# Performance work log

Measured on AMD Instinct MI355X. Metric: run time of the kernel, lower is better.

## Reference

```python
import jax, jax.numpy as jnp
import numpy as np

B, S, H, NH, NKV, HD, E, I = 1, 2048, 1024, 16, 8, 64, 8, 2048
TOPK = 2
EPS = 1e-6
THETA = 1e6


def setup_inputs() -> dict:
    key = jax.random.key(0)
    ks = jax.random.split(key, 12)
    init = lambda k, shp: jax.random.normal(k, shp, jnp.float32) * 0.02
    hidden_states = jax.random.normal(ks[0], (B, S, H), jnp.float32)
    attention_mask = jnp.ones((B, S), jnp.float32)
    position_ids = jnp.broadcast_to(jnp.arange(S, dtype=jnp.int32), (B, S))
    inv_freq = 1.0 / (THETA ** (jnp.arange(0, HD, 2, dtype=jnp.float32) / HD))
    freqs = jnp.outer(jnp.arange(S, dtype=jnp.float32), inv_freq)  # [S, HD/2]
    emb = jnp.concatenate([freqs, freqs], axis=-1)                  # [S, HD]
    return dict(
        hidden_states=hidden_states,
        attention_mask=attention_mask,
        position_ids=position_ids,
        sin=jnp.sin(emb), cos=jnp.cos(emb),
        wq=init(ks[1], (H, NH * HD)),
        wk=init(ks[2], (H, NKV * HD)),
        wv=init(ks[3], (H, NKV * HD)),
        wo=init(ks[4], (NH * HD, H)),
        ln1=jnp.ones((H,), jnp.float32),
        ln2=jnp.ones((H,), jnp.float32),
        gate_w=init(ks[5], (H, E)),
        w1=init(ks[6], (E, H, I)),
        w3=init(ks[7], (E, H, I)),
        w2=init(ks[8], (E, I, H)),
    )


def _rms_norm(x, w):
    return x * jax.lax.rsqrt(jnp.mean(jnp.square(x), -1, keepdims=True) + EPS) * w


def _rotate_half(x):
    h = x.shape[-1] // 2
    return jnp.concatenate([-x[..., h:], x[..., :h]], axis=-1)


def reference(hidden_states, attention_mask, position_ids, sin, cos,
              wq, wk, wv, wo, ln1, ln2, gate_w, w1, w3, w2):
    x = hidden_states
    # ---- self-attention block ----
    h = _rms_norm(x, ln1)
    q = (h @ wq).reshape(B, S, NH, HD).transpose(0, 2, 1, 3)    # [B,NH,S,HD]
    k = (h @ wk).reshape(B, S, NKV, HD).transpose(0, 2, 1, 3)   # [B,NKV,S,HD]
    v = (h @ wv).reshape(B, S, NKV, HD).transpose(0, 2, 1, 3)
    sb = sin[position_ids][:, None]  # [B,1,S,HD]
    cb = cos[position_ids][:, None]
    q = q * cb + _rotate_half(q) * sb
    k = k * cb + _rotate_half(k) * sb
    rep = NH // NKV
    k = jnp.repeat(k, rep, axis=1)  # GQA repeat -> [B,NH,S,HD]
    v = jnp.repeat(v, rep, axis=1)
    causal = jnp.tril(jnp.ones((S, S), bool))
    mask = causal[None, None] & (attention_mask[:, None, None, :] > 0)
    bias = jnp.where(mask, 0.0, jnp.finfo(jnp.float32).min)
    scale = 1.0 / jnp.sqrt(jnp.float32(HD))
    scores = jnp.einsum('bhqd,bhkd->bhqk', q, k) * scale + bias
    attn = jax.nn.softmax(scores, axis=-1)
    o = jnp.einsum('bhqk,bhkd->bhqd', attn, v)
    o = o.transpose(0, 2, 1, 3).reshape(B, S, NH * HD) @ wo
    x = x + o
    # ---- sparse MoE block (top-2 of E experts, SiLU-gated MLP) ----
    t = _rms_norm(x, ln2).reshape(B * S, H)
    router_logits = t @ gate_w                         # [T,E]
    probs = jax.nn.softmax(router_logits, axis=-1)
    top_w, top_i = jax.lax.top_k(probs, TOPK)          # [T,2]
    top_w = top_w / jnp.sum(top_w, axis=-1, keepdims=True)
    full_w = jnp.sum(jax.nn.one_hot(top_i, E, dtype=t.dtype) * top_w[..., None], axis=1)  # [T,E]
    moe_out = jnp.zeros_like(t)
    for e in range(E):  # fixed small expert count
        ge = jax.nn.silu(t @ w1[e]) * (t @ w3[e])      # [T,I]
        moe_out = moe_out + full_w[:, e:e + 1] * (ge @ w2[e])
    x = x + moe_out.reshape(B, S, H)
    return x
```

## Files before the change

### kernel.cpp

```cpp
#include <hip/hip_runtime.h>

#define S 2048
#define H 1024
#define NH 16
#define NKV 8
#define HD 64
#define NE 8
#define ID 2048

typedef short bf16x8 __attribute__((ext_vector_type(8)));
typedef short bf16x4 __attribute__((ext_vector_type(4)));
typedef float f32x4 __attribute__((ext_vector_type(4)));

__device__ __forceinline__ unsigned short f2bf(float f) {
  unsigned u = __builtin_bit_cast(unsigned, f);
  u += 0x7FFFu + ((u >> 16) & 1u);
  return (unsigned short)(u >> 16);
}
__device__ __forceinline__ float bf2f(unsigned short h) {
  unsigned u = ((unsigned)h) << 16;
  return __builtin_bit_cast(float, u);
}
__device__ __forceinline__ unsigned cvtpk(float a, float b) {
  unsigned r;
// ... 17 lines not shown
  const float* sb = src + (size_t)(kt * 128) * N + nt * 64 + ln;
#pragma unroll 8
  for (int rr = 0; rr < 32; rr++) {
    int r = rr * 4 + wv;
    tile[r][ln] = sb[(size_t)r * N];
  }
  __syncthreads();
  int seg = tid & 15;
  int rq = tid >> 4;
#pragma unroll
  for (int it = 0; it < 4; it++) {
    int row = it * 16 + rq;
    int cs = seg * 8;
    size_t dbase = (size_t)(nt * 64 + row) * K + kt * 128 + cs;
    unsigned short th[8], tl[8];
#pragma unroll
    for (int i = 0; i < 8; i++) {
      float vv = tile[cs + i][row];
      unsigned short h_ = f2bf(vv);
      th[i] = h_;
      if (LO) tl[i] = f2bf(vv - bf2f(h_));
    }
    *(bf16x8*)(hi + dbase) = *(bf16x8*)&th[0];
    if (LO) *(bf16x8*)(lo + dbase) = *(bf16x8*)&tl[0];
  }
}

__global__ __launch_bounds__(256) void prep_kernel(
    const float* __restrict__ x, const float* __restrict__ ln1,
    unsigned short* __restrict__ h_hi, unsigned short* __restrict__ h_lo,
    const float* __restrict__ wq, const float* __restrict__ wk, const float* __restrict__ wv,
    const float* __restrict__ wo, unsigned short* __restrict__ wqkvT_hi,
    unsigned short* __restrict__ wqkvT_lo, unsigned short* __restrict__ woT_hi,
    unsigned short* __restrict__ woT_lo) {
  __shared__ float tile[128][65];
  __shared__ float part[4];
  int u = blockIdx.x, grp = u / 19, slot = u % 19;
  int tid = threadIdx.x;
  if (slot < 16) {
    int row = grp * 16 + slot;
    const float* xr = x + (size_t)row * H;
    float v[4];
    float ss = 0.f;
#pragma unroll
    for (int i = 0; i < 4; i++) {
      v[i] = xr[tid + i * 256];
      ss += v[i] * v[i];
    }
#pragma unroll
    for (int off = 1; off < 64; off <<= 1) ss += __shfl_xor(ss, off);
    if ((tid & 63) == 0) part[tid >> 6] = ss;
    __syncthreads();
    float tot = part[0] + part[1] + part[2] + part[3];
    float r = rsqrtf(tot * (1.f / H) + 1e-6f);
#pragma unroll
    for (int i = 0; i < 4; i++) {
      int c = tid + i * 256;
      float vv = v[i] * r * ln1[c];
      size_t o = (size_t)row * H + c;
      unsigned short h_ = f2bf(vv);
      h_hi[o] = h_;
      h_lo[o] = f2bf(vv - bf2f(h_));
    }
  } else {
    int local = grp * 3 + (slot - 16);
    const float* src;
    unsigned short *hi, *lo;
    int N, l2;
    if (local < 128) {
      src = wq; hi = wqkvT_hi; lo = wqkvT_lo; N = 1024; l2 = local;
    } else if (local < 192) {
      src = wk; hi = wqkvT_hi + (size_t)1024 * 1024; lo = wqkvT_lo + (size_t)1024 * 1024; N = 512; l2 = local - 128;
    } else if (local < 256) {
      src = wv; hi = wqkvT_hi + (size_t)1536 * 1024; lo = wqkvT_lo + (size_t)1536 * 1024; N = 512; l2 = local - 192;
    } else {
      src = wo; hi = woT_hi; lo = woT_lo; N = 1024; l2 = local - 256;
    }
    int ntc = N >> 6;
    int nt = l2 % ntc, kt = l2 / ntc;
    tconv_tile128<true>(src, hi, lo, 1024, N, nt, kt, tile);
  }
}

__global__ __launch_bounds__(256) void rv_kernel(
    const float* __restrict__ qkv, const float* __restrict__ sinb,
    const float* __restrict__ cosb, const int* __restrict__ pos,
    unsigned short* __restrict__ qhi, unsigned short* __restrict__ qlo,
    unsigned short* __restrict__ khi, unsigned short* __restrict__ klo,
    unsigned short* __restrict__ vThi, unsigned short* __restrict__ vTlo) {
  __shared__ float tile[64][65];
  int u = blockIdx.x, grp = u / 25, slot = u % 25;
  int tid = threadIdx.x;
  if (slot == 0) {
    int st = grp & 31, hk = grp >> 5;
    int r = tid >> 2, seg = (tid & 3) * 16;
    const float* src = qkv + (size_t)(st * 64 + r) * 2048 + 1536 + hk * HD + seg;
#pragma unroll
    for (int i = 0; i < 16; i += 4) {
      float4 a = *(const float4*)(src + i);
      tile[r][seg + i] = a.x;
      tile[r][seg + i + 1] = a.y;
      tile[r][seg + i + 2] = a.z;
      tile[r][seg + i + 3] = a.w;
    }
    __syncthreads();
    int d = tid >> 2, ss = (tid & 3) * 16;
    unsigned short th[16], tl[16];
#pragma unroll
    for (int i = 0; i < 16; i++) {
      float vv = tile[ss + i][d];
      unsigned short h_ = f2bf(vv);
      th[i] = h_;
      tl[i] = f2bf(vv - bf2f(h_));
    }
    size_t dst = ((size_t)hk * HD + d) * S + st * 64 + ss;
    *(bf16x8*)(vThi + dst) = *(bf16x8*)&th[0];
    *(bf16x8*)(vThi + dst + 8) = *(bf16x8*)&th[8];
    *(bf16x8*)(vTlo + dst) = *(bf16x8*)&tl[0];
    *(bf16x8*)(vTlo + dst + 8) = *(bf16x8*)&tl[8];
  } else {
    int i = (grp * 24 + slot - 1) * 256 + tid;
    int d = i & 31;
    int s = (i >> 5) & 2047;
    int hh = i >> 16;
    int p = pos[s];
    float c0 = cosb[p * HD + d], c1 = cosb[p * HD + d + 32];
    float s0 = sinb[p * HD + d], s1 = sinb[p * HD + d + 32];
    const float* srcb = qkv + (size_t)s * 2048;
    if (hh < NH) {
      float x0 = srcb[hh * HD + d], x1 = srcb[hh * HD + d + 32];
      float r0 = (x0 * c0 - x1 * s0) * 0.125f;
      float r1 = (x1 * c1 + x0 * s1) * 0.125f;
      size_t o = ((size_t)hh * S + s) * HD + d;
      unsigned short h0 = f2bf(r0), h1 = f2bf(r1);
      qhi[o] = h0;
      qlo[o] = f2bf(r0 - bf2f(h0));
      qhi[o + 32] = h1;
      qlo[o + 32] = f2bf(r1 - bf2f(h1));
    } else {
      int hk = hh - NH;
      float x0 = srcb[1024 + hk * HD + d], x1 = srcb[1024 + hk * HD + d + 32];
      float r0 = x0 * c0 - x1 * s0;
      float r1 = x1 * c1 + x0 * s1;
      size_t o = ((size_t)hk * S + s) * HD + d;
      unsigned short h0 = f2bf(r0), h1 = f2bf(r1);
      khi[o] = h0;
      klo[o] = f2bf(r0 - bf2f(h0));
      khi[o + 32] = h1;
      klo[o + 32] = f2bf(r1 - bf2f(h1));
    }
  }
}

__global__ __launch_bounds__(256, 4) void gemm1_w13_kernel(
    const unsigned short* __restrict__ oh, const unsigned short* __restrict__ ol,
    const unsigned short* __restrict__ woh, const unsigned short* __restrict__ wol,
    float* __restrict__ x2, float* __restrict__ out, const float* __restrict__ resid,
    const float* __restrict__ w1, const float* __restrict__ w3,
    unsigned short* __restrict__ w1T, unsigned short* __restrict__ w3T) {
  __shared__ __align__(16) char smem[33280];
  int u = blockIdx.x, grp = u / 9, slot = u % 9;
  int tid = threadIdx.x;
  if (slot != 0) {
    int t = grp * 8 + slot - 1;
    int b = t >> 8, rem = t & 255, kt = rem >> 5, nt = rem & 31;
    const float* src = (b < 8) ? w1 + (size_t)b * 1024 * 2048 : w3 + (size_t)(b - 8) * 1024 * 2048;
    unsigned short* hi = (b < 8) ? w1T + (size_t)b * 2048 * 1024 : w3T + (size_t)(b - 8) * 2048 * 1024;
    tconv_tile128<false>(src, hi, nullptr, 1024, 2048, nt, kt, (float(*)[65])smem);
    return;
  }
  int g = grp;
  int bx = g & 15, by = g >> 4;
  unsigned short* tAh = (unsigned short*)smem;
  unsigned short* tAl = tAh + 4096;
  unsigned short* tBh = tAl + 4096;
  unsigned short* tBl = tBh + 4096;
  int n0 = bx * 64, m0 = by * 64;
  int w = tid >> 6, lane = tid & 63;
  int lr = lane & 15, gq = lane >> 4;
  int rloc = lane >> 3, slotg = (lane & 7) ^ rloc;
  int wm = w >> 1, wn = w & 1;
  unsigned aOff[2], bOff[2];
#pragma unroll
  for (int cc = 0; cc < 2; cc++) {
    int rr = (w * 2 + cc) * 8 + rloc;
    aOff[cc] = (unsigned)((m0 + rr) * 1024 + slotg * 8);
    bOff[cc] = (unsigned)((n0 + rr) * 1024 + slotg * 8);
  }
  f32x4 acc[2][2];
#pragma unroll
  for (int i = 0; i < 2; i++)
#pragma unroll
    for (int j = 0; j < 2; j++) acc[i][j] = f32x4{0.f, 0.f, 0.f, 0.f};
  for (int k0 = 0; k0 < 1024; k0 += 64) {
    __syncthreads();
#pragma unroll
    for (int cc = 0; cc < 2; cc++) {
      int cb = (w * 2 + cc) * 512;
      gload16(oh + aOff[cc] + k0, &tAh[cb]);
      gload16(ol + aOff[cc] + k0, &tAl[cb]);
      gload16(woh + bOff[cc] + k0, &tBh[cb]);
      gload16(wol + bOff[cc] + k0, &tBl[cb]);
    }
    __syncthreads();
    bf16x8 fah[2][2], fal[2][2];
#pragma unroll
    for (int i = 0; i < 2; i++) {
      int ar = wm * 32 + i * 16 + lr;
#pragma unroll
      for (int kk = 0; kk < 2; kk++) {
        int off = ar * 64 + (((kk * 4 + gq) ^ (ar & 7)) * 8);
        fah[i][kk] = *(const bf16x8*)&tAh[off];
        fal[i][kk] = *(const bf16x8*)&tAl[off];
      }
    }
#pragma unroll
    for (int j = 0; j < 2; j++) {
      int br = wn * 32 + j * 16 + lr;
      bf16x8 fbh[2], fbl[2];
#pragma unroll
      for (int kk = 0; kk < 2; kk++) {
        int off = br * 64 + (((kk * 4 + gq) ^ (br & 7)) * 8);
        fbh[kk] = *(const bf16x8*)&tBh[off];
        fbl[kk] = *(const bf16x8*)&tBl[off];
      }
#pragma unroll
      for (int i = 0; i < 2; i++) {
#pragma unroll
        for (int kk = 0; kk < 2; kk++) {
          acc[i][j] = __builtin_amdgcn_mfma_f32_16x16x32_bf16(fah[i][kk], fbh[kk], acc[i][j], 0, 0, 0);
          acc[i][j] = __builtin_amdgcn_mfma_f32_16x16x32_bf16(fah[i][kk], fbl[kk], acc[i][j], 0, 0, 0);
          acc[i][j] = __builtin_amdgcn_mfma_f32_16x16x32_bf16(fal[i][kk], fbh[kk], acc[i][j], 0, 0, 0);
        }
      }
    }
  }
#pragma unroll
  for (int i = 0; i < 2; i++)
#pragma unroll
    for (int j = 0; j < 2; j++)
#pragma unroll
      for (int r = 0; r < 4; r++) {
        int grow = wm * 32 + i * 16 + gq * 4 + r;
        int gcol = n0 + wn * 32 + j * 16 + lr;
        float o = acc[i][j][r] + resid[(size_t)(m0 + grow) * 1024 + gcol];
        x2[(size_t)(m0 + grow) * 1024 + gcol] = o;
        out[(size_t)(m0 + grow) * 1024 + gcol] = o;
      }
}

__global__ __launch_bounds__(256) void rmsnorm_router_kernel(
    const float* __restrict__ x, const float* __restrict__ wgt,
    const float* __restrict__ gw, unsigned short* __restrict__ ohi,
    int* __restrict__ selE, float* __restrict__ selW) {
  int row = blockIdx.x;
  const float* xr = x + (size_t)row * H;
  int tid = threadIdx.x;
  float v[4];
  float ss = 0.f;
#pragma unroll
  for (int i = 0; i < 4; i++) {
    v[i] = xr[tid + i * 256];
    ss += v[i] * v[i];
  }
#pragma unroll
  for (int off = 1; off < 64; off <<= 1) ss += __shfl_xor(ss, off);
  __shared__ float part[4];
  __shared__ float red[4][NE];
  if ((tid & 63) == 0) part[tid >> 6] = ss;
  __syncthreads();
  float tot = part[0] + part[1] + part[2] + part[3];
  float r = rsqrtf(tot * (1.f / H) + 1e-6f);
  float acc[NE];
#pragma unroll
  for (int e = 0; e < NE; e++) acc[e] = 0.f;
#pragma unroll
  for (int i = 0; i < 4; i++) {
    int c = tid + i * 256;
    float vv = v[i] * r * wgt[c];
    ohi[(size_t)row * H + c] = f2bf(vv);
    const float4* gp = (const float4*)(gw + (size_t)c * NE);
    float4 g0 = gp[0], g1 = gp[1];
    acc[0] += vv * g0.x;
    acc[1] += vv * g0.y;
    acc[2] += vv * g0.z;
    acc[3] += vv * g0.w;
    acc[4] += vv * g1.x;
    acc[5] += vv * g1.y;
    acc[6] += vv * g1.z;
    acc[7] += vv * g1.w;
  }
#pragma unroll
  for (int off = 1; off < 64; off <<= 1) {
#pragma unroll
    for (int e = 0; e < NE; e++) acc[e] += __shfl_xor(acc[e], off);
  }
  if ((tid & 63) == 0) {
#pragma unroll
    for (int e = 0; e < NE; e++) red[tid >> 6][e] = acc[e];
  }
  __syncthreads();
  if (tid == 0) {
    float lg[NE];
#pragma unroll
    for (int e = 0; e < NE; e++) lg[e] = red[0][e] + red[1][e] + red[2][e] + red[3][e];
    int e1 = 0;
#pragma unroll
    for (int e = 1; e < NE; e++)
      if (lg[e] > lg[e1]) e1 = e;
    int e2 = -1;
#pragma unroll
    for (int e = 0; e < NE; e++)
      if (e != e1 && (e2 < 0 || lg[e] > lg[e2])) e2 = e;
    float w1v = 1.f / (1.f + __expf(lg[e2] - lg[e1]));
    selE[row] = e1 | (e2 << 8);
    selW[row * 2] = w1v;
    selW[row * 2 + 1] = 1.f - w1v;
  }
}

__global__ __launch_bounds__(256) void assign_kernel(const int* __restrict__ selE,
                                                     int* __restrict__ cnt,
                                                     int* __restrict__ offs,
                                                     int* __restrict__ tmap,
                                                     int* __restrict__ idxb,
                                                     int* __restrict__ tokslot) {
  int tid = threadIdx.x;
  __shared__ int sc[256][NE];
  int pack[8];
// ... 94 lines not shown
template <int MODE>
__global__ __launch_bounds__(256, 4) void gemm_kernel(
    const unsigned short* __restrict__ Ah, const unsigned short* __restrict__ Al,
    const unsigned short* __restrict__ Bh, const unsigned short* __restrict__ Bl,
    float* __restrict__ C, unsigned short* __restrict__ Gout,
    const int* __restrict__ idx, const int* __restrict__ cnt, const int* __restrict__ offs,
    const int* __restrict__ tmap, int N, int K) {
  constexpr int BM = (MODE <= 1) ? 64 : 128;
  constexpr int NI = BM / 32;
  int n0 = blockIdx.x * 64, m0, e = 0;
  int ce = 0, gbase = 0;
  if (MODE >= 2) {
    int ntiles = tmap[63];
    if ((int)blockIdx.y >= ntiles) return;
    int packed = tmap[blockIdx.y];
    e = packed >> 16;
    m0 = (packed & 0xffff) * 128;
    ce = cnt[e];
    gbase = offs[e];
  } else {
    m0 = blockIdx.y * BM;
  }
  const unsigned short* bhp = Bh;
  const unsigned short* blp = Bl;
  if (MODE == 2) {
    bhp += (size_t)e * 2048 * 1024;
    blp += (size_t)e * 2048 * 1024;
  }
  if (MODE == 3) bhp += (size_t)e * 1024 * 2048;

  __shared__ __align__(16) unsigned short tAh[BM * 64];
  __shared__ __align__(16) unsigned short tAl[MODE <= 1 ? BM * 64 : 8];
  __shared__ __align__(16) unsigned short tBh[64 * 64];
  __shared__ __align__(16) unsigned short tBl[MODE <= 2 ? 64 * 64 : 8];

  int tid = threadIdx.x, w = tid >> 6, lane = tid & 63;
  int lr = lane & 15, g = lane >> 4;
  int rloc = lane >> 3, slotg = (lane & 7) ^ rloc;
  int wm = w >> 1, wn = w & 1;

  unsigned aOff[NI], bOff[2];
#pragma unroll
  for (int cc = 0; cc < NI; cc++) {
    int rr = (w * NI + cc) * 8 + rloc;
    if (MODE == 2) {
      int gr = m0 + rr;
      if (gr > ce - 1) gr = ce - 1;
      int tok = idx[e * S + gr];
      aOff[cc] = (unsigned)(tok * K + slotg * 8);
    } else if (MODE == 3) {
      int gr = gbase + m0 + rr;
      if (gr > 4095) gr = 4095;
      aOff[cc] = (unsigned)(gr * K + slotg * 8);
    } else {
      aOff[cc] = (unsigned)((m0 + rr) * K + slotg * 8);
    }
  }
#pragma unroll
  for (int cc = 0; cc < 2; cc++) {
    int rr = (w * 2 + cc) * 8 + rloc;
    bOff[cc] = (unsigned)((n0 + rr) * K + slotg * 8);
  }

  f32x4 acc[NI][2], acc2[NI][2];
#pragma unroll
  for (int i = 0; i < NI; i++)
#pragma unroll
    for (int j = 0; j < 2; j++) {
      acc[i][j] = f32x4{0.f, 0.f, 0.f, 0.f};
      if (MODE == 2) acc2[i][j] = f32x4{0.f, 0.f, 0.f, 0.f};
    }

  int kbeg = 0, kend = K;
  if (MODE == 3) {
    kbeg = (int)blockIdx.z * (K >> 1);
    kend = kbeg + (K >> 1);
  }
  for (int k0 = kbeg; k0 < kend; k0 += 64) {
    __syncthreads();
#pragma unroll
    for (int cc = 0; cc < NI; cc++) {
      int cb = (w * NI + cc) * 512;
      gload16(Ah + aOff[cc] + k0, &tAh[cb]);
      if (MODE <= 1) gload16(Al + aOff[cc] + k0, &tAl[cb]);
    }
#pragma unroll
    for (int cc = 0; cc < 2; cc++) {
      int cb = (w * 2 + cc) * 512;
      gload16(bhp + bOff[cc] + k0, &tBh[cb]);
      if (MODE <= 2) gload16(blp + bOff[cc] + k0, &tBl[cb]);
    }
    __syncthreads();
    bf16x8 fah[NI][2], fal[NI][2];
#pragma unroll
    for (int i = 0; i < NI; i++) {
      int ar = wm * (BM / 2) + i * 16 + lr;
#pragma unroll
      for (int kk = 0; kk < 2; kk++) {
        int off = ar * 64 + (((kk * 4 + g) ^ (ar & 7)) * 8);
        fah[i][kk] = *(const bf16x8*)&tAh[off];
        if (MODE <= 1) fal[i][kk] = *(const bf16x8*)&tAl[off];
      }
    }
#pragma unroll
    for (int j = 0; j < 2; j++) {
      int br = wn * 32 + j * 16 + lr;
      bf16x8 fbh[2], fbl[2];
#pragma unroll
      for (int kk = 0; kk < 2; kk++) {
        int off = br * 64 + (((kk * 4 + g) ^ (br & 7)) * 8);
        fbh[kk] = *(const bf16x8*)&tBh[off];
        if (MODE <= 2) fbl[kk] = *(const bf16x8*)&tBl[off];
      }
#pragma unroll
      for (int i = 0; i < NI; i++) {
#pragma unroll
        for (int kk = 0; kk < 2; kk++) {
          acc[i][j] = __builtin_amdgcn_mfma_f32_16x16x32_bf16(fah[i][kk], fbh[kk], acc[i][j], 0, 0, 0);
          if (MODE <= 1) {
            acc[i][j] = __builtin_amdgcn_mfma_f32_16x16x32_bf16(fah[i][kk], fbl[kk], acc[i][j], 0, 0, 0);
            acc[i][j] = __builtin_amdgcn_mfma_f32_16x16x32_bf16(fal[i][kk], fbh[kk], acc[i][j], 0, 0, 0);
          }
          if (MODE == 2)
            acc2[i][j] = __builtin_amdgcn_mfma_f32_16x16x32_bf16(fah[i][kk], fbl[kk], acc2[i][j], 0, 0, 0);
        }
      }
    }
  }
#pragma unroll
  for (int i = 0; i < NI; i++)
#pragma unroll
    for (int j = 0; j < 2; j++)
#pragma unroll
      for (int r = 0; r < 4; r++) {
        int grow = wm * (BM / 2) + i * 16 + g * 4 + r;
        int gcol = n0 + wn * 32 + j * 16 + lr;
        float v = acc[i][j][r];
        if (MODE == 0) {
          C[(size_t)(m0 + grow) * N + gcol] = v;
        } else if (MODE == 2) {
          if (m0 + grow < ce) {
            float g3 = acc2[i][j][r];
            float sg = v / (1.f + __expf(-v));
            Gout[(size_t)(gbase + m0 + grow) * 2048 + gcol] = f2bf(sg * g3);
          }
        } else if (MODE == 3) {
          if (m0 + grow < ce) {
            C[(size_t)blockIdx.z * 4096 * 1024 + (size_t)(gbase + m0 + grow) * 1024 + gcol] = v;
          }
        }
      }
}

#define FSWZ(row, byteoff) ((byteoff) ^ (((row) & 7) << 4))

__global__ __launch_bounds__(256, 4) void flash_kernel(
    const unsigned short* __restrict__ qhi, const unsigned short* __restrict__ qlo,
    const unsigned short* __restrict__ khip, const unsigned short* __restrict__ klop,
    const unsigned short* __restrict__ vthip, const unsigned short* __restrict__ vtlop,
    const float* __restrict__ amask, float* __restrict__ po, float* __restrict__ pm,
    float* __restrict__ pl) {
  int u = blockIdx.x;
  int r_ = u >> 8, base = u & 255;
  int qt = (base + r_ * 8) & 31;
  int head = ((base >> 5) & 7) | ((r_ & 1) << 3);
  int z = r_ >> 1;
  int tid = threadIdx.x;
  int w = tid >> 6, lane = tid & 63;
  int lr = lane & 15, g = lane >> 4;
  int rloc = lane >> 3, slotg = (lane & 7) ^ rloc;

  __shared__ __align__(16) unsigned short Khi[64 * 64];
  __shared__ __align__(16) unsigned short Klo[64 * 64];
  __shared__ __align__(16) unsigned short Vhi[64 * 64];
  __shared__ __align__(16) unsigned short Vlo[64 * 64];
  __shared__ __align__(16) unsigned short Pbuf[4][16 * 64];

  int qrow = qt * 64 + w * 16 + lr;
  bf16x8 qh[2], ql[2];
  {
    const unsigned short* qb = qhi + ((size_t)head * S + qrow) * HD;
    const unsigned short* qb2 = qlo + ((size_t)head * S + qrow) * HD;
    qh[0] = *(const bf16x8*)(qb + g * 8);
    qh[1] = *(const bf16x8*)(qb + 32 + g * 8);
    ql[0] = *(const bf16x8*)(qb2 + g * 8);
    ql[1] = *(const bf16x8*)(qb2 + 32 + g * 8);
  }

  f32x4 oacc[4];
#pragma unroll
  for (int dg = 0; dg < 4; dg++) oacc[dg] = f32x4{0.f, 0.f, 0.f, 0.f};
  float m = -1e30f, l = 0.f;

  const unsigned short* kbh = khip + (size_t)(head >> 1) * S * HD;
  const unsigned short* kbl = klop + (size_t)(head >> 1) * S * HD;
  const unsigned short* vbh = vthip + (size_t)(head >> 1) * HD * S;
  const unsigned short* vbl = vtlop + (size_t)(head >> 1) * HD * S;
  char* pbase = (char*)Pbuf[w];

  int nblk = qt + 1;
  int b0 = (z * nblk) >> 1, b1 = ((z + 1) * nblk) >> 1;

  for (int kb = b0; kb < b1; kb++) {
    int kv0 = kb * 64;
    __syncthreads();
#pragma unroll
    for (int cc = 0; cc < 2; cc++) {
      int c = w * 2 + cc;
      int r = c * 8 + rloc;
      gload16(kbh + (size_t)(kv0 + r) * HD + slotg * 8, &Khi[c * 512]);
      gload16(kbl + (size_t)(kv0 + r) * HD + slotg * 8, &Klo[c * 512]);
      gload16(vbh + (size_t)r * S + kv0 + slotg * 8, &Vhi[c * 512]);
      gload16(vbl + (size_t)r * S + kv0 + slotg * 8, &Vlo[c * 512]);
    }
    unsigned long long vm = __ballot(amask[kv0 + lane] > 0.f);
    __syncthreads();

    f32x4 sacc[4];
#pragma unroll
    for (int c = 0; c < 4; c++) sacc[c] = f32x4{0.f, 0.f, 0.f, 0.f};
#pragma unroll
    for (int c = 0; c < 4; c++) {
#pragma unroll
      for (int kc = 0; kc < 2; kc++) {
        int row = c * 16 + lr;
        int bo = FSWZ(row, row * 128 + kc * 64 + g * 16);
        bf16x8 khf = *(const bf16x8*)((char*)Khi + bo);
        bf16x8 klf = *(const bf16x8*)((char*)Klo + bo);
        sacc[c] = __builtin_amdgcn_mfma_f32_16x16x32_bf16(khf, qh[kc], sacc[c], 0, 0, 0);
        sacc[c] = __builtin_amdgcn_mfma_f32_16x16x32_bf16(khf, ql[kc], sacc[c], 0, 0, 0);
        sacc[c] = __builtin_amdgcn_mfma_f32_16x16x32_bf16(klf, qh[kc], sacc[c], 0, 0, 0);
      }
    }
    int qloc = w * 16 + lr;
    bool diag = (kb == qt);
    bool fullvis = (vm == ~0ull) && !diag;
    float tm = -1e30f;
    if (fullvis) {
#pragma unroll
      for (int c = 0; c < 4; c++)
#pragma unroll
        for (int r = 0; r < 4; r++) tm = fmaxf(tm, sacc[c][r]);
    } else {
#pragma unroll
      for (int c = 0; c < 4; c++) {
#pragma unroll
        for (int r = 0; r < 4; r++) {
          int kvloc = c * 16 + 4 * g + r;
          bool vis = ((vm >> kvloc) & 1ull) && (!diag || kvloc <= qloc);
          float sv = vis ? sacc[c][r] : -1e30f;
          sacc[c][r] = sv;
          tm = fmaxf(tm, sv);
        }
      }
    }
    tm = fmaxf(tm, __shfl_xor(tm, 16));
    tm = fmaxf(tm, __shfl_xor(tm, 32));
    bool skip = __all(tm - m <= 8.f);
    float newm = skip ? m : fmaxf(m, tm);
    float rs = 0.f;
#pragma unroll
    for (int c = 0; c < 4; c++) {
#pragma unroll
      for (int r = 0; r < 4; r++) {
        float p = __expf(sacc[c][r] - newm);
        sacc[c][r] = p;
        rs += p;
      }
    }
    rs += __shfl_xor(rs, 16);
    rs += __shfl_xor(rs, 32);
    if (!skip) {
      float alpha = __expf(m - newm);
      m = newm;
      l = l * alpha + rs;
#pragma unroll
      for (int dg = 0; dg < 4; dg++) {
#pragma unroll
        for (int r = 0; r < 4; r++) oacc[dg][r] *= alpha;
      }
    } else {
      l += rs;
    }
    unsigned hw[4][2];
#pragma unroll
    for (int c = 0; c < 4; c++) {
      hw[c][0] = cvtpk(sacc[c][0], sacc[c][1]);
      hw[c][1] = cvtpk(sacc[c][2], sacc[c][3]);
      uint2 hv = {hw[c][0], hw[c][1]};
      *(uint2*)(pbase + FSWZ(lr, lr * 128 + (c * 16 + 4 * g) * 2)) = hv;
    }
    bf16x8 pbh[2], pbl[2];
#pragma unroll
    for (int kc = 0; kc < 2; kc++)
      pbh[kc] = *(const bf16x8*)(pbase + FSWZ(lr, lr * 128 + kc * 64 + g * 16));
#pragma unroll
    for (int c = 0; c < 4; c++) {
      float h0 = __builtin_bit_cast(float, hw[c][0] << 16);
      float h1 = __builtin_bit_cast(float, hw[c][0] & 0xffff0000u);
      float h2 = __builtin_bit_cast(float, hw[c][1] << 16);
      float h3 = __builtin_bit_cast(float, hw[c][1] & 0xffff0000u);
      uint2 lv = {cvtpk(sacc[c][0] - h0, sacc[c][1] - h1),
                  cvtpk(sacc[c][2] - h2, sacc[c][3] - h3)};
      *(uint2*)(pbase + FSWZ(lr, lr * 128 + (c * 16 + 4 * g) * 2)) = lv;
    }
#pragma unroll
    for (int kc = 0; kc < 2; kc++)
      pbl[kc] = *(const bf16x8*)(pbase + FSWZ(lr, lr * 128 + kc * 64 + g * 16));
#pragma unroll
    for (int dg = 0; dg < 4; dg++) {
#pragma unroll
      for (int kc = 0; kc < 2; kc++) {
        int row = dg * 16 + lr;
        int bo = FSWZ(row, row * 128 + kc * 64 + g * 16);
        bf16x8 vhf = *(const bf16x8*)((char*)Vhi + bo);
        bf16x8 vlf = *(const bf16x8*)((char*)Vlo + bo);
        oacc[dg] = __builtin_amdgcn_mfma_f32_16x16x32_bf16(vhf, pbh[kc], oacc[dg], 0, 0, 0);
        oacc[dg] = __builtin_amdgcn_mfma_f32_16x16x32_bf16(vhf, pbl[kc], oacc[dg], 0, 0, 0);
        oacc[dg] = __builtin_amdgcn_mfma_f32_16x16x32_bf16(vlf, pbh[kc], oacc[dg], 0, 0, 0);
      }
    }
  }

  size_t pb = (size_t)(qt * 16 + head) * 2 + z;
  int row = w * 16 + lr;
  if (g == 0) {
    pm[pb * 64 + row] = m;
    pl[pb * 64 + row] = l;
  }
  float* pob = po + pb * 4096 + (size_t)row * 64;
#pragma unroll
  for (int dg = 0; dg < 4; dg++) {
    float4 v4 = {oacc[dg][0], oacc[dg][1], oacc[dg][2], oacc[dg][3]};
    *(float4*)(pob + dg * 16 + 4 * g) = v4;
  }
}

__global__ __launch_bounds__(256) void combine_kernel(const float* __restrict__ po,
                                                      const float* __restrict__ pm,
                                                      const float* __restrict__ pl,
                                                      unsigned short* __restrict__ ohi,
                                                      unsigned short* __restrict__ olo) {
  int qt = blockIdx.x, head = blockIdx.y;
  int r = threadIdx.x >> 2, dg = (threadIdx.x & 3) * 16;
  size_t base = (size_t)(qt * 16 + head) * 2;
  float m0v = pm[base * 64 + r], m1v = pm[(base + 1) * 64 + r];
  float l0 = pl[base * 64 + r], l1 = pl[(base + 1) * 64 + r];
  float M = fmaxf(m0v, m1v);
  float w0 = __expf(m0v - M), w1 = __expf(m1v - M);
  float inv = 1.f / (w0 * l0 + w1 * l1);
  const float* p0 = po + base * 4096 + (size_t)r * 64 + dg;
  const float* p1 = po + (base + 1) * 4096 + (size_t)r * 64 + dg;
  unsigned short th[16], tl[16];
#pragma unroll
  for (int i = 0; i < 16; i += 4) {
    float4 a = *(const float4*)(p0 + i);
    float4 b = *(const float4*)(p1 + i);
    float vv[4] = {(w0 * a.x + w1 * b.x) * inv, (w0 * a.y + w1 * b.y) * inv,
                   (w0 * a.z + w1 * b.z) * inv, (w0 * a.w + w1 * b.w) * inv};
#pragma unroll
    for (int j = 0; j < 4; j++) {
      unsigned short h_ = f2bf(vv[j]);
      th[i + j] = h_;
      tl[i + j] = f2bf(vv[j] - bf2f(h_));
    }
  }
  size_t ob = (size_t)(qt * 64 + r) * 1024 + head * 64 + dg;
  *(bf16x8*)(ohi + ob) = *(bf16x8*)&th[0];
  *(bf16x8*)(ohi + ob + 8) = *(bf16x8*)&th[8];
  *(bf16x8*)(olo + ob) = *(bf16x8*)&tl[0];
  *(bf16x8*)(olo + ob + 8) = *(bf16x8*)&tl[8];
}

extern "C" void kernel_launch(void* const* d_in, const int* in_sizes, int n_in,
                              void* d_out, int out_size, void* d_ws, size_t ws_size,
                              hipStream_t stream) {
  const float* x = (const float*)d_in[0];
  const float* amask = (const float*)d_in[1];
  const int* pos = (const int*)d_in[2];
  const float* sinb = (const float*)d_in[3];
  const float* cosb = (const float*)d_in[4];
  const float* wq = (const float*)d_in[5];
  const float* wk = (const float*)d_in[6];
  const float* wv = (const float*)d_in[7];
  const float* wo = (const float*)d_in[8];
  const float* ln1 = (const float*)d_in[9];
  const float* ln2 = (const float*)d_in[10];
  const float* gw = (const float*)d_in[11];
  const float* w1 = (const float*)d_in[12];
  const float* w3 = (const float*)d_in[13];
  const float* w2 = (const float*)d_in[14];
  float* out = (float*)d_out;

  char* ws = (char*)d_ws;
  const size_t MB = 1024 * 1024;
  float* x2 = (float*)(ws + 0 * MB);
  unsigned short* t_bf = (unsigned short*)(ws + 8 * MB);
  int* cnt = (int*)(ws + 12 * MB);
  int* offs = cnt + 16;
  int* tmap = cnt + 32;
  int* idxb = cnt + 128;
  int* selE = idxb + 16384;
  int* tokslot = selE + 2048;
  float* selW = (float*)(tokslot + 4096);
  unsigned short* o_hi = (unsigned short*)(ws + 13 * MB);
  unsigned short* o_lo = (unsigned short*)(ws + 17 * MB);
  unsigned short* G = (unsigned short*)(ws + 13 * MB);
  float* qkv = (float*)(ws + 13 * MB);
  unsigned short* w1T = (unsigned short*)(ws + 29 * MB);
  unsigned short* w3T = (unsigned short*)(ws + 61 * MB);
  unsigned short* w2T = (unsigned short*)(ws + 29 * MB);
  float* moeP = (float*)(ws + 61 * MB);
  float* po = (float*)(ws + 29 * MB);
  float* pm = (float*)(ws + 45 * MB);
  float* pl = (float*)(ws + 46 * MB);
  unsigned short* wqkvT_hi = (unsigned short*)(ws + 47 * MB);
  unsigned short* wqkvT_lo = (unsigned short*)(ws + 51 * MB);
  unsigned short* h_hi = (unsigned short*)(ws + 55 * MB);
  unsigned short* h_lo = (unsigned short*)(ws + 59 * MB);
  unsigned short* q_hi = (unsigned short*)(ws + 63 * MB);
  unsigned short* q_lo = (unsigned short*)(ws + 67 * MB);
  unsigned short* k_hi = (unsigned short*)(ws + 71 * MB);
  unsigned short* k_lo = (unsigned short*)(ws + 73 * MB);
  unsigned short* vT_hi = (unsigned short*)(ws + 75 * MB);
  unsigned short* vT_lo = (unsigned short*)(ws + 77 * MB);
  unsigned short* woT_hi = (unsigned short*)(ws + 93 * MB);
  unsigned short* woT_lo = (unsigned short*)(ws + 95 * MB);

  prep_kernel<<<2432, 256, 0, stream>>>(x, ln1, h_hi, h_lo, wq, wk, wv, wo, wqkvT_hi, wqkvT_lo,
                                        woT_hi, woT_lo);
  gemm_kernel<0><<<dim3(32, 32, 1), 256, 0, stream>>>(h_hi, h_lo, wqkvT_hi, wqkvT_lo, qkv, nullptr,
                                                      nullptr, nullptr, nullptr, nullptr, 2048,
                                                      1024);
  rv_kernel<<<6400, 256, 0, stream>>>(qkv, sinb, cosb, pos, q_hi, q_lo, k_hi, k_lo, vT_hi, vT_lo);
  flash_kernel<<<dim3(1024, 1, 1), 256, 0, stream>>>(q_hi, q_lo, k_hi, k_lo, vT_hi, vT_lo, amask,
                                                     po, pm, pl);
  combine_kernel<<<dim3(32, 16), 256, 0, stream>>>(po, pm, pl, o_hi, o_lo);
  gemm1_w13_kernel<<<4608, 256, 0, stream>>>(o_hi, o_lo, woT_hi, woT_lo, x2, out, x, w1, w3, w1T,
                                             w3T);
  rmsnorm_router_kernel<<<S, 256, 0, stream>>>(x2, ln2, gw, t_bf, selE, selW);
  assign_kernel<<<1, 256, 0, stream>>>(selE, cnt, offs, tmap, idxb, tokslot);
  gemm_kernel<2><<<dim3(32, 40, 1), 256, 0, stream>>>(t_bf, nullptr, w1T, w3T, nullptr, G, idxb,
                                                      cnt, offs, tmap, 2048, 1024);
  tconv_w2_kernel<<<dim3(16, 16, 8), 256, 0, stream>>>(w2, w2T);
  gemm_kernel<3><<<dim3(16, 40, 2), 256, 0, stream>>>(G, nullptr, w2T, nullptr, moeP, nullptr,
                                                      idxb, cnt, offs, tmap, 1024, 2048);
  moe_gather_kernel<<<S, 256, 0, stream>>>(moeP, tokslot, selW, out);
}
```

Before: 281.3 us.

## Co-schedule w1/w3 weight transpose with flash attention instead of output GEMM

Moves the w1/w3 fp32-to-bf16 transpose tiles out of the output-projection GEMM launch and interleaves them with flash-attention blocks (4 transpose blocks per attention block). The goal is to fill idle CU time from causal-attention imbalance with memory-bound conversion work, leaving the Wo GEMM as a lean 512-block launch. The workspace is remapped so w1T/w3T no longer overlap the attention partials. The attention MFMA loops also gain s_setprio hints. The risk is that the bandwidth-heavy transpose competes with attention's loads and that the shared-memory footprint per block grows.

```diff
diff --git a/kernel.cpp b/kernel.cpp
--- a/kernel.cpp
+++ b/kernel.cpp
@@ -193,29 +193,215 @@
   }
 }
 
-__global__ __launch_bounds__(256, 4) void gemm1_w13_kernel(
-    const unsigned short* __restrict__ oh, const unsigned short* __restrict__ ol,
-    const unsigned short* __restrict__ woh, const unsigned short* __restrict__ wol,
-    float* __restrict__ x2, float* __restrict__ out, const float* __restrict__ resid,
-    const float* __restrict__ w1, const float* __restrict__ w3,
+#define FSWZ(row, byteoff) ((byteoff) ^ (((row) & 7) << 4))
+
+__global__ __launch_bounds__(256, 4) void flash_w13_kernel(
+    const unsigned short* __restrict__ qhi, const unsigned short* __restrict__ qlo,
+    const unsigned short* __restrict__ khip, const unsigned short* __restrict__ klop,
+    const unsigned short* __restrict__ vthip, const unsigned short* __restrict__ vtlop,
+    const float* __restrict__ amask, float* __restrict__ po, float* __restrict__ pm,
+    float* __restrict__ pl, const float* __restrict__ w1, const float* __restrict__ w3,
     unsigned short* __restrict__ w1T, unsigned short* __restrict__ w3T) {
-  __shared__ __align__(16) char smem[33280];
-  int u = blockIdx.x, grp = u / 9, slot = u % 9;
+  __shared__ __align__(16) char smem[40960];
+  int uu = blockIdx.x, grp = uu / 5, slot = uu % 5;
   int tid = threadIdx.x;
   if (slot != 0) {
-    int t = grp * 8 + slot - 1;
+    int t = grp * 4 + slot - 1;
     int b = t >> 8, rem = t & 255, kt = rem >> 5, nt = rem & 31;
     const float* src = (b < 8) ? w1 + (size_t)b * 1024 * 2048 : w3 + (size_t)(b - 8) * 1024 * 2048;
     unsigned short* hi = (b < 8) ? w1T + (size_t)b * 2048 * 1024 : w3T + (size_t)(b - 8) * 2048 * 1024;
     tconv_tile128<false>(src, hi, nullptr, 1024, 2048, nt, kt, (float(*)[65])smem);
     return;
   }
-  int g = grp;
+  unsigned short* Khi = (unsigned short*)smem;
+  unsigned short* Klo = Khi + 4096;
+  unsigned short* Vhi = Klo + 4096;
+  unsigned short* Vlo = Vhi + 4096;
+  unsigned short* Pbuf = Vlo + 4096;
+  int u = grp;
+  int r_ = u >> 8, base = u & 255;
+  int qt = (base + r_ * 8) & 31;
+  int head = ((base >> 5) & 7) | ((r_ & 1) << 3);
+  int z = r_ >> 1;
+  int w = tid >> 6, lane = tid & 63;
+  int lr = lane & 15, g = lane >> 4;
+  int rloc = lane >> 3, slotg = (lane & 7) ^ rloc;
+
+  int qrow = qt * 64 + w * 16 + lr;
+  bf16x8 qh[2], ql[2];
+  {
+    const unsigned short* qb = qhi + ((size_t)head * S + qrow) * HD;
+    const unsigned short* qb2 = qlo + ((size_t)head * S + qrow) * HD;
+    qh[0] = *(const bf16x8*)(qb + g * 8);
+    qh[1] = *(const bf16x8*)(qb + 32 + g * 8);
+    ql[0] = *(const bf16x8*)(qb2 + g * 8);
+    ql[1] = *(const bf16x8*)(qb2 + 32 + g * 8);
+  }
+
+  f32x4 oacc[4];
+#pragma unroll
+  for (int dg = 0; dg < 4; dg++) oacc[dg] = f32x4{0.f, 0.f, 0.f, 0.f};
+  float m = -1e30f, l = 0.f;
+
+  const unsigned short* kbh = khip + (size_t)(head >> 1) * S * HD;
+  const unsigned short* kbl = klop + (size_t)(head >> 1) * S * HD;
+  const unsigned short* vbh = vthip + (size_t)(head >> 1) * HD * S;
+  const unsigned short* vbl = vtlop + (size_t)(head >> 1) * HD * S;
+  char* pbase = (char*)(Pbuf + w * 1024);
+
+  int nblk = qt + 1;
+  int b0 = (z * nblk) >> 1, b1 = ((z + 1) * nblk) >> 1;
+
+  for (int kb = b0; kb < b1; kb++) {
+    int kv0 = kb * 64;
+    __syncthreads();
+#pragma unroll
+    for (int cc = 0; cc < 2; cc++) {
+      int c = w * 2 + cc;
+      int r = c * 8 + rloc;
+      gload16(kbh + (size_t)(kv0 + r) * HD + slotg * 8, &Khi[c * 512]);
+      gload16(kbl + (size_t)(kv0 + r) * HD + slotg * 8, &Klo[c * 512]);
+      gload16(vbh + (size_t)r * S + kv0 + slotg * 8, &Vhi[c * 512]);
+      gload16(vbl + (size_t)r * S + kv0 + slotg * 8, &Vlo[c * 512]);
+    }
+    unsigned long long vm = __ballot(amask[kv0 + lane] > 0.f);
+    __syncthreads();
+
+    f32x4 sacc[4];
+#pragma unroll
+    for (int c = 0; c < 4; c++) sacc[c] = f32x4{0.f, 0.f, 0.f, 0.f};
+    __builtin_amdgcn_s_setprio(1);
+#pragma unroll
+    for (int c = 0; c < 4; c++) {
+#pragma unroll
+      for (int kc = 0; kc < 2; kc++) {
+        int row = c * 16 + lr;
+        int bo = FSWZ(row, row * 128 + kc * 64 + g * 16);
+        bf16x8 khf = *(const bf16x8*)((char*)Khi + bo);
+        bf16x8 klf = *(const bf16x8*)((char*)Klo + bo);
+        sacc[c] = __builtin_amdgcn_mfma_f32_16x16x32_bf16(khf, qh[kc], sacc[c], 0, 0, 0);
+        sacc[c] = __builtin_amdgcn_mfma_f32_16x16x32_bf16(khf, ql[kc], sacc[c], 0, 0, 0);
+        sacc[c] = __builtin_amdgcn_mfma_f32_16x16x32_bf16(klf, qh[kc], sacc[c], 0, 0, 0);
+      }
+    }
+    __builtin_amdgcn_s_setprio(0);
+    int qloc = w * 16 + lr;
+    bool diag = (kb == qt);
+    bool fullvis = (vm == ~0ull) && !diag;
+    float tm = -1e30f;
+    if (fullvis) {
+#pragma unroll
+      for (int c = 0; c < 4; c++)
+#pragma unroll
+        for (int r = 0; r < 4; r++) tm = fmaxf(tm, sacc[c][r]);
+    } else {
+#pragma unroll
+      for (int c = 0; c < 4; c++) {
+#pragma unroll
+        for (int r = 0; r < 4; r++) {
+          int kvloc = c * 16 + 4 * g + r;
+          bool vis = ((vm >> kvloc) & 1ull) && (!diag || kvloc <= qloc);
+          float sv = vis ? sacc[c][r] : -1e30f;
+          sacc[c][r] = sv;
+          tm = fmaxf(tm, sv);
+        }
+      }
+    }
+    tm = fmaxf(tm, __shfl_xor(tm, 16));
+    tm = fmaxf(tm, __shfl_xor(tm, 32));
+    bool skip = __all(tm - m <= 8.f);
+    float newm = skip ? m : fmaxf(m, tm);
+    float rs = 0.f;
+#pragma unroll
+    for (int c = 0; c < 4; c++) {
+#pragma unroll
+      for (int r = 0; r < 4; r++) {
+        float p = __expf(sacc[c][r] - newm);
+        sacc[c][r] = p;
+        rs += p;
+      }
+    }
+    rs += __shfl_xor(rs, 16);
+    rs += __shfl_xor(rs, 32);
+    if (!skip) {
+      float alpha = __expf(m - newm);
+      m = newm;
+      l = l * alpha + rs;
+#pragma unroll
+      for (int dg = 0; dg < 4; dg++) {
+#pragma unroll
+        for (int r = 0; r < 4; r++) oacc[dg][r] *= alpha;
+      }
+    } else {
+      l += rs;
+    }
+    unsigned hw[4][2];
+#pragma unroll
+    for (int c = 0; c < 4; c++) {
+      hw[c][0] = cvtpk(sacc[c][0], sacc[c][1]);
+      hw[c][1] = cvtpk(sacc[c][2], sacc[c][3]);
+      uint2 hv = {hw[c][0], hw[c][1]};
+      *(uint2*)(pbase + FSWZ(lr, lr * 128 + (c * 16 + 4 * g) * 2)) = hv;
+    }
+    bf16x8 pbh[2], pbl[2];
+#pragma unroll
+    for (int kc = 0; kc < 2; kc++)
+      pbh[kc] = *(const bf16x8*)(pbase + FSWZ(lr, lr * 128 + kc * 64 + g * 16));
+#pragma unroll
+    for (int c = 0; c < 4; c++) {
+      float h0 = __builtin_bit_cast(float, hw[c][0] << 16);
+      float h1 = __builtin_bit_cast(float, hw[c][0] & 0xffff0000u);
+      float h2 = __builtin_bit_cast(float, hw[c][1] << 16);
+      float h3 = __builtin_bit_cast(float, hw[c][1] & 0xffff0000u);
+      uint2 lv = {cvtpk(sacc[c][0] - h0, sacc[c][1] - h1),
+                  cvtpk(sacc[c][2] - h2, sacc[c][3] - h3)};
+      *(uint2*)(pbase + FSWZ(lr, lr * 128 + (c * 16 + 4 * g) * 2)) = lv;
+    }
+#pragma unroll
+    for (int kc = 0; kc < 2; kc++)
+      pbl[kc] = *(const bf16x8*)(pbase + FSWZ(lr, lr * 128 + kc * 64 + g * 16));
+    __builtin_amdgcn_s_setprio(1);
+#pragma unroll
+    for (int dg = 0; dg < 4; dg++) {
+#pragma unroll
+      for (int kc = 0; kc < 2; kc++) {
+        int row = dg * 16 + lr;
+        int bo = FSWZ(row, row * 128 + kc * 64 + g * 16);
+        bf16x8 vhf = *(const bf16x8*)((char*)Vhi + bo);
+        bf16x8 vlf = *(const bf16x8*)((char*)Vlo + bo);
+        oacc[dg] = __builtin_amdgcn_mfma_f32_16x16x32_bf16(vhf, pbh[kc], oacc[dg], 0, 0, 0);
+        oacc[dg] = __builtin_amdgcn_mfma_f32_16x16x32_bf16(vhf, pbl[kc], oacc[dg], 0, 0, 0);
+        oacc[dg] = __builtin_amdgcn_mfma_f32_16x16x32_bf16(vlf, pbh[kc], oacc[dg], 0, 0, 0);
+      }
+    }
+    __builtin_amdgcn_s_setprio(0);
+  }
+
+  size_t pb = (size_t)(qt * 16 + head) * 2 + z;
+  int row = w * 16 + lr;
+  if (g == 0) {
+    pm[pb * 64 + row] = m;
+    pl[pb * 64 + row] = l;
+  }
+  float* pob = po + pb * 4096 + (size_t)row * 64;
+#pragma unroll
+  for (int dg = 0; dg < 4; dg++) {
+    float4 v4 = {oacc[dg][0], oacc[dg][1], oacc[dg][2], oacc[dg][3]};
+    *(float4*)(pob + dg * 16 + 4 * g) = v4;
+  }
+}
+
+__global__ __launch_bounds__(256, 4) void gemm1_kernel(
+    const unsigned short* __restrict__ oh, const unsigned short* __restrict__ ol,
+    const unsigned short* __restrict__ woh, const unsigned short* __restrict__ wol,
+    float* __restrict__ x2, float* __restrict__ out, const float* __restrict__ resid) {
+  __shared__ __align__(16) unsigned short tAh[4096];
+  __shared__ __align__(16) unsigned short tAl[4096];
+  __shared__ __align__(16) unsigned short tBh[4096];
+  __shared__ __align__(16) unsigned short tBl[4096];
+  int g = blockIdx.x;
   int bx = g & 15, by = g >> 4;
-  unsigned short* tAh = (unsigned short*)smem;
-  unsigned short* tAl = tAh + 4096;
-  unsigned short* tBh = tAl + 4096;
-  unsigned short* tBl = tBh + 4096;
+  int tid = threadIdx.x;
   int n0 = bx * 64, m0 = by * 64;
   int w = tid >> 6, lane = tid & 63;
   int lr = lane & 15, gq = lane >> 4;
@@ -616,190 +802,6 @@
       }
 }
 
-#define FSWZ(row, byteoff) ((byteoff) ^ (((row) & 7) << 4))
-
-__global__ __launch_bounds__(256, 4) void flash_kernel(
-    const unsigned short* __restrict__ qhi, const unsigned short* __restrict__ qlo,
-    const unsigned short* __restrict__ khip, const unsigned short* __restrict__ klop,
-    const unsigned short* __restrict__ vthip, const unsigned short* __restrict__ vtlop,
-    const float* __restrict__ amask, float* __restrict__ po, float* __restrict__ pm,
-    float* __restrict__ pl) {
-  int u = blockIdx.x;
-  int r_ = u >> 8, base = u & 255;
-  int qt = (base + r_ * 8) & 31;
-  int head = ((base >> 5) & 7) | ((r_ & 1) << 3);
-  int z = r_ >> 1;
-  int tid = threadIdx.x;
-  int w = tid >> 6, lane = tid & 63;
-  int lr = lane & 15, g = lane >> 4;
-  int rloc = lane >> 3, slotg = (lane & 7) ^ rloc;
-
-  __shared__ __align__(16) unsigned short Khi[64 * 64];
-  __shared__ __align__(16) unsigned short Klo[64 * 64];
-  __shared__ __align__(16) unsigned short Vhi[64 * 64];
-  __shared__ __align__(16) unsigned short Vlo[64 * 64];
-  __shared__ __align__(16) unsigned short Pbuf[4][16 * 64];
-
-  int qrow = qt * 64 + w * 16 + lr;
-  bf16x8 qh[2], ql[2];
-  {
-    const unsigned short* qb = qhi + ((size_t)head * S + qrow) * HD;
-    const unsigned short* qb2 = qlo + ((size_t)head * S + qrow) * HD;
-    qh[0] = *(const bf16x8*)(qb + g * 8);
-    qh[1] = *(const bf16x8*)(qb + 32 + g * 8);
-    ql[0] = *(const bf16x8*)(qb2 + g * 8);
-    ql[1] = *(const bf16x8*)(qb2 + 32 + g * 8);
-  }
-
-  f32x4 oacc[4];
-#pragma unroll
-  for (int dg = 0; dg < 4; dg++) oacc[dg] = f32x4{0.f, 0.f, 0.f, 0.f};
-  float m = -1e30f, l = 0.f;
-
-  const unsigned short* kbh = khip + (size_t)(head >> 1) * S * HD;
-  const unsigned short* kbl = klop + (size_t)(head >> 1) * S * HD;
-  const unsigned short* vbh = vthip + (size_t)(head >> 1) * HD * S;
-  const unsigned short* vbl = vtlop + (size_t)(head >> 1) * HD * S;
-  char* pbase = (char*)Pbuf[w];
-
-  int nblk = qt + 1;
-  int b0 = (z * nblk) >> 1, b1 = ((z + 1) * nblk) >> 1;
-
-  for (int kb = b0; kb < b1; kb++) {
-    int kv0 = kb * 64;
-    __syncthreads();
-#pragma unroll
-    for (int cc = 0; cc < 2; cc++) {
-      int c = w * 2 + cc;
-      int r = c * 8 + rloc;
-      gload16(kbh + (size_t)(kv0 + r) * HD + slotg * 8, &Khi[c * 512]);
-      gload16(kbl + (size_t)(kv0 + r) * HD + slotg * 8, &Klo[c * 512]);
-      gload16(vbh + (size_t)r * S + kv0 + slotg * 8, &Vhi[c * 512]);
-      gload16(vbl + (size_t)r * S + kv0 + slotg * 8, &Vlo[c * 512]);
-    }
-    unsigned long long vm = __ballot(amask[kv0 + lane] > 0.f);
-    __syncthreads();
-
-    f32x4 sacc[4];
-#pragma unroll
-    for (int c = 0; c < 4; c++) sacc[c] = f32x4{0.f, 0.f, 0.f, 0.f};
-#pragma unroll
-    for (int c = 0; c < 4; c++) {
-#pragma unroll
-      for (int kc = 0; kc < 2; kc++) {
-        int row = c * 16 + lr;
-        int bo = FSWZ(row, row * 128 + kc * 64 + g * 16);
-        bf16x8 khf = *(const bf16x8*)((char*)Khi + bo);
-        bf16x8 klf = *(const bf16x8*)((char*)Klo + bo);
-        sacc[c] = __builtin_amdgcn_mfma_f32_16x16x32_bf16(khf, qh[kc], sacc[c], 0, 0, 0);
-        sacc[c] = __builtin_amdgcn_mfma_f32_16x16x32_bf16(khf, ql[kc], sacc[c], 0, 0, 0);
-        sacc[c] = __builtin_amdgcn_mfma_f32_16x16x32_bf16(klf, qh[kc], sacc[c], 0, 0, 0);
-      }
-    }
-    int qloc = w * 16 + lr;
-    bool diag = (kb == qt);
-    bool fullvis = (vm == ~0ull) && !diag;
-    float tm = -1e30f;
-    if (fullvis) {
-#pragma unroll
-      for (int c = 0; c < 4; c++)
-#pragma unroll
-        for (int r = 0; r < 4; r++) tm = fmaxf(tm, sacc[c][r]);
-    } else {
-#pragma unroll
-      for (int c = 0; c < 4; c++) {
-#pragma unroll
-        for (int r = 0; r < 4; r++) {
-          int kvloc = c * 16 + 4 * g + r;
-          bool vis = ((vm >> kvloc) & 1ull) && (!diag || kvloc <= qloc);
-          float sv = vis ? sacc[c][r] : -1e30f;
-          sacc[c][r] = sv;
-          tm = fmaxf(tm, sv);
-        }
-      }
-    }
-    tm = fmaxf(tm, __shfl_xor(tm, 16));
-    tm = fmaxf(tm, __shfl_xor(tm, 32));
-    bool skip = __all(tm - m <= 8.f);
-    float newm = skip ? m : fmaxf(m, tm);
-    float rs = 0.f;
-#pragma unroll
-    for (int c = 0; c < 4; c++) {
-#pragma unroll
-      for (int r = 0; r < 4; r++) {
-        float p = __expf(sacc[c][r] - newm);
-        sacc[c][r] = p;
-        rs += p;
-      }
-    }
-    rs += __shfl_xor(rs, 16);
-    rs += __shfl_xor(rs, 32);
-    if (!skip) {
-      float alpha = __expf(m - newm);
-      m = newm;
-      l = l * alpha + rs;
-#pragma unroll
-      for (int dg = 0; dg < 4; dg++) {
-#pragma unroll
-        for (int r = 0; r < 4; r++) oacc[dg][r] *= alpha;
-      }
-    } else {
-      l += rs;
-    }
-    unsigned hw[4][2];
-#pragma unroll
-    for (int c = 0; c < 4; c++) {
-      hw[c][0] = cvtpk(sacc[c][0], sacc[c][1]);
-      hw[c][1] = cvtpk(sacc[c][2], sacc[c][3]);
-      uint2 hv = {hw[c][0], hw[c][1]};
-      *(uint2*)(pbase + FSWZ(lr, lr * 128 + (c * 16 + 4 * g) * 2)) = hv;
-    }
-    bf16x8 pbh[2], pbl[2];
-#pragma unroll
-    for (int kc = 0; kc < 2; kc++)
-      pbh[kc] = *(const bf16x8*)(pbase + FSWZ(lr, lr * 128 + kc * 64 + g * 16));
-#pragma unroll
-    for (int c = 0; c < 4; c++) {
-      float h0 = __builtin_bit_cast(float, hw[c][0] << 16);
-      float h1 = __builtin_bit_cast(float, hw[c][0] & 0xffff0000u);
-      float h2 = __builtin_bit_cast(float, hw[c][1] << 16);
-      float h3 = __builtin_bit_cast(float, hw[c][1] & 0xffff0000u);
-      uint2 lv = {cvtpk(sacc[c][0] - h0, sacc[c][1] - h1),
-                  cvtpk(sacc[c][2] - h2, sacc[c][3] - h3)};
-      *(uint2*)(pbase + FSWZ(lr, lr * 128 + (c * 16 + 4 * g) * 2)) = lv;
-    }
-#pragma unroll
-    for (int kc = 0; kc < 2; kc++)
-      pbl[kc] = *(const bf16x8*)(pbase + FSWZ(lr, lr * 128 + kc * 64 + g * 16));
-#pragma unroll
-    for (int dg = 0; dg < 4; dg++) {
-#pragma unroll
-      for (int kc = 0; kc < 2; kc++) {
-        int row = dg * 16 + lr;
-        int bo = FSWZ(row, row * 128 + kc * 64 + g * 16);
-        bf16x8 vhf = *(const bf16x8*)((char*)Vhi + bo);
-        bf16x8 vlf = *(const bf16x8*)((char*)Vlo + bo);
-        oacc[dg] = __builtin_amdgcn_mfma_f32_16x16x32_bf16(vhf, pbh[kc], oacc[dg], 0, 0, 0);
-        oacc[dg] = __builtin_amdgcn_mfma_f32_16x16x32_bf16(vhf, pbl[kc], oacc[dg], 0, 0, 0);
-        oacc[dg] = __builtin_amdgcn_mfma_f32_16x16x32_bf16(vlf, pbh[kc], oacc[dg], 0, 0, 0);
-      }
-    }
-  }
-
-  size_t pb = (size_t)(qt * 16 + head) * 2 + z;
-  int row = w * 16 + lr;
-  if (g == 0) {
-    pm[pb * 64 + row] = m;
-    pl[pb * 64 + row] = l;
-  }
-  float* pob = po + pb * 4096 + (size_t)row * 64;
-#pragma unroll
-  for (int dg = 0; dg < 4; dg++) {
-    float4 v4 = {oacc[dg][0], oacc[dg][1], oacc[dg][2], oacc[dg][3]};
-    *(float4*)(pob + dg * 16 + 4 * g) = v4;
-  }
-}
-
 __global__ __launch_bounds__(256) void combine_kernel(const float* __restrict__ po,
                                                       const float* __restrict__ pm,
                                                       const float* __restrict__ pl,
@@ -858,6 +860,7 @@
 
   char* ws = (char*)d_ws;
   const size_t MB = 1024 * 1024;
+  const size_t KB = 1024;
   float* x2 = (float*)(ws + 0 * MB);
   unsigned short* t_bf = (unsigned short*)(ws + 8 * MB);
   int* cnt = (int*)(ws + 12 * MB);
@@ -867,29 +870,32 @@
   int* selE = idxb + 16384;
   int* tokslot = selE + 2048;
   float* selW = (float*)(tokslot + 4096);
-  unsigned short* o_hi = (unsigned short*)(ws + 13 * MB);
-  unsigned short* o_lo = (unsigned short*)(ws + 17 * MB);
+  float* pm = (float*)(ws + 12 * MB + 512 * KB);
+  float* pl = (float*)(ws + 12 * MB + 768 * KB);
+  float* qkv = (float*)(ws + 13 * MB);
+  float* po = (float*)(ws + 13 * MB);
   unsigned short* G = (unsigned short*)(ws + 13 * MB);
-  float* qkv = (float*)(ws + 13 * MB);
   unsigned short* w1T = (unsigned short*)(ws + 29 * MB);
   unsigned short* w3T = (unsigned short*)(ws + 61 * MB);
   unsigned short* w2T = (unsigned short*)(ws + 29 * MB);
   float* moeP = (float*)(ws + 61 * MB);
-  float* po = (float*)(ws + 29 * MB);
-  float* pm = (float*)(ws + 45 * MB);
-  float* pl = (float*)(ws + 46 * MB);
-  unsigned short* wqkvT_hi = (unsigned short*)(ws + 47 * MB);
-  unsigned short* wqkvT_lo = (unsigned short*)(ws + 51 * MB);
-  unsigned short* h_hi = (unsigned short*)(ws + 55 * MB);
-  unsigned short* h_lo = (unsigned short*)(ws + 59 * MB);
-  unsigned short* q_hi = (unsigned short*)(ws + 63 * MB);
-  unsigned short* q_lo = (unsigned short*)(ws + 67 * MB);
-  unsigned short* k_hi = (unsigned short*)(ws + 71 * MB);
-  unsigned short* k_lo = (unsigned short*)(ws + 73 * MB);
-  unsigned short* vT_hi = (unsigned short*)(ws + 75 * MB);
-  unsigned short* vT_lo = (unsigned short*)(ws + 77 * MB);
-  unsigned short* woT_hi = (unsigned short*)(ws + 93 * MB);
-  unsigned short* woT_lo = (unsigned short*)(ws + 95 * MB);
+  unsigned short* wqkvT_hi = (unsigned short*)(ws + 0 * MB);
+  unsigned short* wqkvT_lo = (unsigned short*)(ws + 4 * MB);
+  unsigned short* h_hi = (unsigned short*)(ws + 8 * MB);
+  unsigned short* h_lo = (unsigned short*)(ws + 93 * MB);
+  unsigned short* woT_hi = (unsigned short*)(ws + 29 * MB);
+  unsigned short* woT_lo = (unsigned short*)(ws + 31 * MB);
+  woT_hi = (unsigned short*)(ws + 97 * MB);
+  woT_lo = (unsigned short*)(ws + 99 * MB);
+  unsigned short* q_hi = (unsigned short*)(ws + 101 * MB);
+  unsigned short* q_lo = (unsigned short*)(ws + 105 * MB);
+  unsigned short* k_hi = (unsigned short*)(ws + 109 * MB);
+  unsigned short* k_lo = (unsigned short*)(ws + 111 * MB);
+  unsigned short* vT_hi = (unsigned short*)(ws + 113 * MB);
+  unsigned short* vT_lo = (unsigned short*)(ws + 115 * MB);
+  unsigned short* o_hi = (unsigned short*)(ws + 117 * MB);
+  unsigned short* o_lo = (unsigned short*)(ws + 121 * MB);
+  h_lo = (unsigned short*)(ws + 125 * MB);
 
   prep_kernel<<<2432, 256, 0, stream>>>(x, ln1, h_hi, h_lo, wq, wk, wv, wo, wqkvT_hi, wqkvT_lo,
                                         woT_hi, woT_lo);
@@ -897,11 +903,10 @@
                                                       nullptr, nullptr, nullptr, nullptr, 2048,
                                                       1024);
   rv_kernel<<<6400, 256, 0, stream>>>(qkv, sinb, cosb, pos, q_hi, q_lo, k_hi, k_lo, vT_hi, vT_lo);
-  flash_kernel<<<dim3(1024, 1, 1), 256, 0, stream>>>(q_hi, q_lo, k_hi, k_lo, vT_hi, vT_lo, amask,
-                                                     po, pm, pl);
+  flash_w13_kernel<<<5120, 256, 0, stream>>>(q_hi, q_lo, k_hi, k_lo, vT_hi, vT_lo, amask, po, pm,
+                                             pl, w1, w3, w1T, w3T);
   combine_kernel<<<dim3(32, 16), 256, 0, stream>>>(po, pm, pl, o_hi, o_lo);
-  gemm1_w13_kernel<<<4608, 256, 0, stream>>>(o_hi, o_lo, woT_hi, woT_lo, x2, out, x, w1, w3, w1T,
-                                             w3T);
+  gemm1_kernel<<<512, 256, 0, stream>>>(o_hi, o_lo, woT_hi, woT_lo, x2, out, x);
   rmsnorm_router_kernel<<<S, 256, 0, stream>>>(x2, ln2, gw, t_bf, selE, selW);
   assign_kernel<<<1, 256, 0, stream>>>(selE, cnt, offs, tmap, idxb, tokslot);
   gemm_kernel<2><<<dim3(32, 40, 1), 256, 0, stream>>>(t_bf, nullptr, w1T, w3T, nullptr, G, idxb,
```

Result: slower. 288.6 us (+2.6%).
